# Kernel tuning notes

Hardware: AMD Instinct MI355X
Metric: run time of the kernel (lower is better)

The kernel has to match this reference:

```python
import jax, jax.numpy as jnp
import numpy as np

N_QUBITS = 12
LAYERS = 2
DEPTH = 6
MULTIPLIER = np.pi - np.finfo(np.float32).eps
C = jnp.complex64

# CNOT as a (2,2,2,2) tensor: out[c',t',c,t]
CNOT = jnp.array([[1, 0, 0, 0],
                  [0, 1, 0, 0],
                  [0, 0, 0, 1],
                  [0, 0, 1, 0]], dtype=C).reshape(2, 2, 2, 2)


def _ry(t):
    c, s = jnp.cos(t / 2), jnp.sin(t / 2)
    return jnp.stack([jnp.stack([c, -s]), jnp.stack([s, c])]).astype(C)


def _rz(t):
    e = jnp.exp(-0.5j * t)
    z = jnp.zeros((), C)
    return jnp.stack([jnp.stack([e, z]), jnp.stack([z, jnp.conj(e)])])


def _rot(phi, theta, omega):
    # PennyLane Rot(phi, theta, omega) = RZ(omega) @ RY(theta) @ RZ(phi)
    return _rz(omega) @ _ry(theta) @ _rz(phi)


def _apply_1q(psi, U, w):
    psi = jnp.tensordot(U, psi, axes=([1], [w]))
    return jnp.moveaxis(psi, 0, w)


def _apply_2q(psi, U, c, t):
    psi = jnp.tensordot(U, psi, axes=([2, 3], [c, t]))
    return jnp.moveaxis(psi, (0, 1), (c, t))


def _circuit(x, w):
    # x: (12,) angles; w: (depth, 12, 3) StronglyEntanglingLayers weights
    psi = jnp.zeros((2,) * N_QUBITS, C).at[(0,) * N_QUBITS].set(1.0)
    # AngleEmbedding with rotation='Y'
    for q in range(N_QUBITS):
        psi = _apply_1q(psi, _ry(x[q]), q)
    # StronglyEntanglingLayers: Rot on each wire, then CNOT ring with range r
    depth = w.shape[0]
    for l in range(depth):
        r = l % (N_QUBITS - 1) + 1  # default ranges in PennyLane
        for q in range(N_QUBITS):
            psi = _apply_1q(psi, _rot(w[l, q, 0], w[l, q, 1], w[l, q, 2]), q)
        for q in range(N_QUBITS):
            psi = _apply_2q(psi, CNOT, q, (q + r) % N_QUBITS)
    probs = jnp.real(psi * jnp.conj(psi))  # (2,)*12
    outs = []
    for q in range(N_QUBITS):
        m = probs.sum(axis=tuple(i for i in range(N_QUBITS) if i != q))  # (2,)
        outs.append(m[0] - m[1])  # <Z_q>
    return jnp.stack(outs).astype(jnp.float32)  # (12,)


_vqc = jax.vmap(_circuit, in_axes=(0, None))  # (B,12),(D,12,3) -> (B,12)


def setup_inputs() -> dict:
    key = jax.random.key(0)
    k1, k2 = jax.random.split(key)
    x_ = jax.random.normal(k1, (4096, N_QUBITS), dtype=jnp.float32)
    theta = 0.01 * jax.random.normal(k2, (LAYERS, DEPTH, N_QUBITS, 3), dtype=jnp.float32)
    return {"x_": x_, "theta": theta}


def reference(x_, theta):
    H = x_
    for i in range(theta.shape[0]):
        H = _vqc(H, theta[i])  # (B, 12) expvals, fed back as angles
    return H[:, 3:9] * jnp.float32(MULTIPLIER)
```

## Files before the change

kernel.cpp:

```cpp
#include <hip/hip_runtime.h>
#include <math.h>

#define NQ 12
#define MULT 3.1415925343968237f

typedef _Float16 f16x8 __attribute__((ext_vector_type(8)));
typedef _Float16 f16x2 __attribute__((ext_vector_type(2)));
typedef float f32x4 __attribute__((ext_vector_type(4)));

static __device__ __forceinline__ unsigned int pkh(float a, float b) {
    auto h = __builtin_amdgcn_cvt_pkrtz(a, b);
    return __builtin_bit_cast(unsigned int, h);
}

__host__ __device__ constexpr int cnotf(int s, int r) {
    for (int q = 0; q < NQ; ++q) {
        int tq = q + r; if (tq >= NQ) tq -= NQ;
        s ^= ((s >> (11 - q)) & 1) << (11 - tq);
    }
    return s;
}

__host__ __device__ constexpr int wordL(int I, int u, int n) {
    int I2 = (I >> 2) & 1, I3 = (I >> 3) & 1;
    int u0 = u & 1, u1 = (u >> 1) & 1, u2 = (u >> 2) & 1, u3 = (u >> 3) & 1;
    int n0 = n & 1, n1 = (n >> 1) & 1, n2 = (n >> 2) & 1, n3 = (n >> 3) & 1;
    return (I & 3) | ((I2 ^ u1 ^ n0) << 2) | ((I3 ^ u2 ^ n1) << 3) |
           ((I2 ^ u2 ^ n2) << 4) | (u0 << 5) | (u3 << 6) | (n0 << 7) |
           (n1 << 8) | (n2 << 9) | (n3 << 10) | (u1 << 11);
}

__global__ void vqc_prep(const float* __restrict__ th, _Float16* __restrict__ frag,
                         int* __restrict__ ptabd) {
    int gid = blockIdx.x * 256 + threadIdx.x;
    int job = gid >> 6, lane = gid & 63;
    if (job < 72) {
        int pg = job >> 1, R = job & 1;
        int layer = pg / 18, rem = pg % 18, depth = rem / 3, ph = rem % 3;
        float g[4][2][2][2];
        for (int j = 0; j < 4; ++j) {
            int q = 4 * ph + j;
            const float* w = th + (((layer * 6 + depth) * 12 + q) * 3);
            float phi = w[0], tht = w[1], om = w[2];
            float st, ct, spo, cpo, smo, cmo;
            sincosf(0.5f * tht, &st, &ct);
            sincosf(0.5f * (phi + om), &spo, &cpo);
            sincosf(0.5f * (phi - om), &smo, &cmo);
            g[j][0][0][0] = ct * cpo;  g[j][0][0][1] = -ct * spo;
            g[j][0][1][0] = -st * cmo; g[j][0][1][1] = -st * smo;
            g[j][1][0][0] = st * cmo;  g[j][1][0][1] = -st * smo;
            g[j][1][1][0] = ct * cpo;  g[j][1][1][1] = ct * spo;
        }
        int m = 16 * R + (lane & 15);
        int u = m >> 1, v = m & 1;
        float Wr[4], Wi[4];
        for (int c = 0; c < 4; ++c) {
            int up = (lane >> 4) * 4 + c;
            float ar = 1.f, ai = 0.f;
            for (int j = 0; j < 4; ++j) {
                int ub = (u >> (3 - j)) & 1, vb = (up >> (3 - j)) & 1;
                float gr = g[j][ub][vb][0], gi = g[j][ub][vb][1];
                float nr = ar * gr - ai * gi, ni = ar * gi + ai * gr;
                ar = nr; ai = ni;
            }
            Wr[c] = ar; Wi[c] = ai;
        }
        _Float16* o = frag + ((size_t)job * 64 + lane) * 8;
        for (int i = 0; i < 8; ++i) {
            int c = i >> 1, vp = i & 1;
            float val = (v == vp) ? Wr[c] : (v == 0 ? -Wi[c] : Wi[c]);
            o[i] = (_Float16)val;
        }
    }
    if (blockIdx.x == 0 && threadIdx.x < 72) {
        int d = threadIdx.x / 12, bb = threadIdx.x % 12;
        int sp = cnotf(1 << bb, d + 1);
        ptabd[threadIdx.x] = wordL((sp >> 8) & 15, sp & 15, (sp >> 4) & 15);
    }
}

__global__ __launch_bounds__(256, 4) void vqc_main(
        const float* __restrict__ x, const uint4* __restrict__ frag,
        const int* __restrict__ ptabd, float* __restrict__ out, int nst) {
    __shared__ __align__(16) unsigned int sbuf[8192];
    __shared__ float ang[64];
    const int t = threadIdx.x, lane = t & 63, wv = t >> 6, b = blockIdx.x;
    if (b >= nst) return;

    const int rbase = wordL(4 * (lane >> 4), 4 * wv, lane & 15);
    const int wbase = wordL(lane & 15, 2 * (lane >> 4), 4 * wv);
    constexpr int RC[4] = {wordL(0,0,0), wordL(0,1,0), wordL(0,2,0), wordL(0,3,0)};
    constexpr int WCt[4] = {wordL(0,0,0), wordL(0,0,1), wordL(0,0,2), wordL(0,0,3)};

    int cur = 0;
    float myang = 0.f;
#pragma unroll 1
    for (int l = 0; l < 2; ++l) {
        if (l == 0) { if (lane < NQ) myang = x[b * NQ + lane]; }
        else        { if (lane < NQ) myang = ang[48 + lane]; }
        float sv, cv;
        sincosf(0.5f * myang, &sv, &cv);
        float cq[NQ], sq[NQ];
#pragma unroll
        for (int q = 0; q < NQ; ++q) { cq[q] = __shfl(cv, q, 64); sq[q] = __shfl(sv, q, 64); }
        __syncthreads();

        {
            float Pn = 1.f;
#pragma unroll
            for (int j = 0; j < 4; ++j) Pn *= ((lane >> j) & 1) ? sq[7 - j] : cq[7 - j];
            float Phi = (((lane >> 4) & 1) ? sq[1] : cq[1]) * (((lane >> 4) & 2) ? sq[0] : cq[0]);
            float pre = Pn * Phi;
            float Plo0 = cq[3] * cq[2], Plo1 = sq[3] * cq[2];
            float Plo2 = cq[3] * sq[2], Plo3 = sq[3] * sq[2];
#pragma unroll
            for (int t2 = 0; t2 < 4; ++t2) {
                float Pu = ((t2 & 1) ? sq[11] : cq[11]) * ((t2 & 2) ? sq[10] : cq[10]) *
                           ((wv & 1) ? sq[9] : cq[9]) * ((wv & 2) ? sq[8] : cq[8]);
                float base = pre * Pu;
                uint4 w;
                w.x = pkh(base * Plo0, 0.f);
                w.y = pkh(base * Plo1, 0.f);
                w.z = pkh(base * Plo2, 0.f);
                w.w = pkh(base * Plo3, 0.f);
                *(uint4*)&sbuf[cur * 4096 + (rbase ^ RC[t2])] = w;
            }
        }
        __syncthreads();

#pragma unroll 1
        for (int d = 0; d < 6; ++d) {
            const int* pdp = ptabd + d * 12;
            int p0 = pdp[0], p1 = pdp[1], p2 = pdp[2], p3 = pdp[3];
            int p4 = pdp[4], p5 = pdp[5], p6 = pdp[6], p7 = pdp[7];
            int p8 = pdp[8], p9 = pdp[9], p10 = pdp[10], p11 = pdp[11];
            int pb = 0;
            if (lane & 1)  pb ^= p8;
            if (lane & 2)  pb ^= p9;
            if (lane & 4)  pb ^= p10;
            if (lane & 8)  pb ^= p11;
            if (lane & 16) pb ^= p1;
            if (lane & 32) pb ^= p2;
            if (wv & 1)    pb ^= p6;
            if (wv & 2)    pb ^= p7;
#pragma unroll
            for (int ph = 0; ph < 3; ++ph) {
                const int pg = (l * 6 + d) * 3 + ph;
                f16x8 a0 = __builtin_bit_cast(f16x8, frag[(pg * 2 + 0) * 64 + lane]);
                f16x8 a1 = __builtin_bit_cast(f16x8, frag[(pg * 2 + 1) * 64 + lane]);
                const unsigned int* rp = sbuf + cur * 4096;
                f32x4 zero = {0.f, 0.f, 0.f, 0.f};
                f32x4 ac[2][4];
#pragma unroll
                for (int t2 = 0; t2 < 4; ++t2) {
                    f16x8 bf = __builtin_bit_cast(f16x8, *(const uint4*)&rp[rbase ^ RC[t2]]);
                    ac[0][t2] = __builtin_amdgcn_mfma_f32_16x16x32_f16(a0, bf, zero, 0, 0, 0);
                    ac[1][t2] = __builtin_amdgcn_mfma_f32_16x16x32_f16(a1, bf, zero, 0, 0, 0);
                }
                unsigned int* wp = sbuf + (cur ^ 1) * 4096;
                if (ph < 2) {
#pragma unroll
                    for (int R = 0; R < 2; ++R)
#pragma unroll
                        for (int t2 = 0; t2 < 4; ++t2)
#pragma unroll
                            for (int pr = 0; pr < 2; ++pr) {
                                int word = wbase ^ (32 * pr + 64 * R) ^ WCt[t2];
                                wp[word] = pkh(ac[R][t2][2 * pr], ac[R][t2][2 * pr + 1]);
                            }
                } else {
#pragma unroll
                    for (int R = 0; R < 2; ++R)
#pragma unroll
                        for (int t2 = 0; t2 < 4; ++t2)
#pragma unroll
                            for (int pr = 0; pr < 2; ++pr) {
                                int sc = (R ? p3 : 0) ^ (pr ? p0 : 0) ^
                                         ((t2 & 1) ? p4 : 0) ^ ((t2 & 2) ? p5 : 0);
                                int word = pb ^ sc;
                                wp[word] = pkh(ac[R][t2][2 * pr], ac[R][t2][2 * pr + 1]);
                            }
                }
                __syncthreads();
                cur ^= 1;
            }
        }

        {
            const unsigned int* rp = sbuf + cur * 4096;
            float P = 0.f, e2 = 0.f, e3 = 0.f, Tt[4];
#pragma unroll
            for (int t2 = 0; t2 < 4; ++t2) {
                uint4 v = *(const uint4*)&rp[rbase ^ RC[t2]];
                unsigned int arr[4] = {v.x, v.y, v.z, v.w};
                float tl = 0.f;
#pragma unroll
                for (int i = 0; i < 4; ++i) {
                    f16x2 h = __builtin_bit_cast(f16x2, arr[i]);
                    float re = (float)h[0], im = (float)h[1];
                    float p = re * re + im * im;
                    tl += p;
                    e2 += (i & 2) ? -p : p;
                    e3 += (i & 1) ? -p : p;
                }
                Tt[t2] = tl; P += tl;
            }
            float r[12];
            r[0] = (lane & 32) ? -P : P;
            r[1] = (lane & 16) ? -P : P;
            r[2] = e2; r[3] = e3;
            r[4] = (lane & 8) ? -P : P;
            r[5] = (lane & 4) ? -P : P;
            r[6] = (lane & 2) ? -P : P;
            r[7] = (lane & 1) ? -P : P;
            r[8] = Tt[0]; r[9] = Tt[1]; r[10] = Tt[2]; r[11] = Tt[3];
#pragma unroll
            for (int k = 0; k < 12; ++k) {
#pragma unroll
                for (int m = 1; m < 64; m <<= 1) r[k] += __shfl_xor(r[k], m, 64);
            }
            if (lane == 0) {
#pragma unroll
                for (int k = 0; k < 12; ++k) ang[wv * 12 + k] = r[k];
            }
            __syncthreads();
            if (t < NQ) {
                float E = 0.f;
                if (t < 8) {
                    E = ang[t] + ang[12 + t] + ang[24 + t] + ang[36 + t];
                } else {
#pragma unroll
                    for (int wvi = 0; wvi < 4; ++wvi)
#pragma unroll
                        for (int t2 = 0; t2 < 4; ++t2) {
                            float v = ang[wvi * 12 + 8 + t2];
                            int Tg = 4 * wvi + t2;
                            int bit = (t == 8) ? ((Tg >> 3) & 1) : (t == 9) ? ((Tg >> 2) & 1)
                                    : (t == 10) ? ((Tg >> 1) & 1) : (Tg & 1);
                            E += bit ? -v : v;
                        }
                }
                if (l == 0) ang[48 + t] = E;
                else if (t >= 3 && t < 9) out[b * 6 + (t - 3)] = E * MULT;
            }
            __syncthreads();
        }
    }
}

extern "C" void kernel_launch(void* const* d_in, const int* in_sizes, int n_in,
                              void* d_out, int out_size, void* d_ws, size_t ws_size,
                              hipStream_t stream) {
    const float* x = (const float*)d_in[0];
    const float* th = (const float*)d_in[1];
    float* outp = (float*)d_out;
    _Float16* fragh = (_Float16*)d_ws;
    int* ptabd = (int*)((char*)d_ws + 73728);

    int batch = in_sizes[0] / NQ;

    hipLaunchKernelGGL(vqc_prep, dim3(18), dim3(256), 0, stream, th, fragh, ptabd);
    hipLaunchKernelGGL(vqc_main, dim3(batch), dim3(256), 0, stream, x,
                       (const uint4*)fragh, ptabd, outp, batch);
}
```

Before: 171.6 us.

## Assign one wavefront per sample to eliminate block-level barriers

Each 64-lane wavefront now simulates a whole 4096-amplitude state by itself, instead of four waves sharing one state. This removes every __syncthreads and the ping-pong double buffer, so the state is updated in place after all 16 chunks are read into registers. The cross-wave reduction through shared memory is replaced by register selects. The cost is 16 KB of LDS per sample and much higher register pressure (ow[16][4] plus the 16 accumulator chunks), which is why launch_bounds drops to 2 blocks per CU. That lowers occupancy and may lengthen each wave's serial critical path.

```diff
diff --git a/kernel.cpp b/kernel.cpp
--- a/kernel.cpp
+++ b/kernel.cpp
@@ -79,31 +79,37 @@
     }
 }
 
-__global__ __launch_bounds__(256, 4) void vqc_main(
+__global__ __launch_bounds__(256, 2) void vqc_main(
         const float* __restrict__ x, const uint4* __restrict__ frag,
         const int* __restrict__ ptabd, float* __restrict__ out, int nst) {
-    __shared__ __align__(16) unsigned int sbuf[8192];
-    __shared__ float ang[64];
-    const int t = threadIdx.x, lane = t & 63, wv = t >> 6, b = blockIdx.x;
+    __shared__ __align__(16) unsigned int sbuf[16384];
+    const int t = threadIdx.x, lane = t & 63, wv = t >> 6;
+    const int b = blockIdx.x * 4 + wv;
     if (b >= nst) return;
-
-    const int rbase = wordL(4 * (lane >> 4), 4 * wv, lane & 15);
-    const int wbase = wordL(lane & 15, 2 * (lane >> 4), 4 * wv);
-    constexpr int RC[4] = {wordL(0,0,0), wordL(0,1,0), wordL(0,2,0), wordL(0,3,0)};
-    constexpr int WCt[4] = {wordL(0,0,0), wordL(0,0,1), wordL(0,0,2), wordL(0,0,3)};
-
-    int cur = 0;
+    unsigned int* sl = sbuf + (wv << 12);
+
+    const int rbase0 = wordL(4 * (lane >> 4), 0, lane & 15);
+    const int wbase0 = wordL(lane & 15, 2 * (lane >> 4), 0);
+    constexpr int UC[16] = {
+        wordL(0,0,0),  wordL(0,1,0),  wordL(0,2,0),  wordL(0,3,0),
+        wordL(0,4,0),  wordL(0,5,0),  wordL(0,6,0),  wordL(0,7,0),
+        wordL(0,8,0),  wordL(0,9,0),  wordL(0,10,0), wordL(0,11,0),
+        wordL(0,12,0), wordL(0,13,0), wordL(0,14,0), wordL(0,15,0)};
+    constexpr int WCN[16] = {
+        wordL(0,0,0),  wordL(0,0,1),  wordL(0,0,2),  wordL(0,0,3),
+        wordL(0,0,4),  wordL(0,0,5),  wordL(0,0,6),  wordL(0,0,7),
+        wordL(0,0,8),  wordL(0,0,9),  wordL(0,0,10), wordL(0,0,11),
+        wordL(0,0,12), wordL(0,0,13), wordL(0,0,14), wordL(0,0,15)};
+
     float myang = 0.f;
 #pragma unroll 1
     for (int l = 0; l < 2; ++l) {
-        if (l == 0) { if (lane < NQ) myang = x[b * NQ + lane]; }
-        else        { if (lane < NQ) myang = ang[48 + lane]; }
+        if (l == 0) myang = (lane < NQ) ? x[b * NQ + lane] : 0.f;
         float sv, cv;
         sincosf(0.5f * myang, &sv, &cv);
         float cq[NQ], sq[NQ];
 #pragma unroll
         for (int q = 0; q < NQ; ++q) { cq[q] = __shfl(cv, q, 64); sq[q] = __shfl(sv, q, 64); }
-        __syncthreads();
 
         {
             float Pn = 1.f;
@@ -114,19 +120,18 @@
             float Plo0 = cq[3] * cq[2], Plo1 = sq[3] * cq[2];
             float Plo2 = cq[3] * sq[2], Plo3 = sq[3] * sq[2];
 #pragma unroll
-            for (int t2 = 0; t2 < 4; ++t2) {
-                float Pu = ((t2 & 1) ? sq[11] : cq[11]) * ((t2 & 2) ? sq[10] : cq[10]) *
-                           ((wv & 1) ? sq[9] : cq[9]) * ((wv & 2) ? sq[8] : cq[8]);
+            for (int c = 0; c < 16; ++c) {
+                float Pu = ((c & 1) ? sq[11] : cq[11]) * ((c & 2) ? sq[10] : cq[10]) *
+                           ((c & 4) ? sq[9] : cq[9]) * ((c & 8) ? sq[8] : cq[8]);
                 float base = pre * Pu;
                 uint4 w;
                 w.x = pkh(base * Plo0, 0.f);
                 w.y = pkh(base * Plo1, 0.f);
                 w.z = pkh(base * Plo2, 0.f);
                 w.w = pkh(base * Plo3, 0.f);
-                *(uint4*)&sbuf[cur * 4096 + (rbase ^ RC[t2])] = w;
-            }
-        }
-        __syncthreads();
+                *(uint4*)&sl[rbase0 ^ UC[c]] = w;
+            }
+        }
 
 #pragma unroll 1
         for (int d = 0; d < 6; ++d) {
@@ -134,64 +139,60 @@
             int p0 = pdp[0], p1 = pdp[1], p2 = pdp[2], p3 = pdp[3];
             int p4 = pdp[4], p5 = pdp[5], p6 = pdp[6], p7 = pdp[7];
             int p8 = pdp[8], p9 = pdp[9], p10 = pdp[10], p11 = pdp[11];
-            int pb = 0;
-            if (lane & 1)  pb ^= p8;
-            if (lane & 2)  pb ^= p9;
-            if (lane & 4)  pb ^= p10;
-            if (lane & 8)  pb ^= p11;
-            if (lane & 16) pb ^= p1;
-            if (lane & 32) pb ^= p2;
-            if (wv & 1)    pb ^= p6;
-            if (wv & 2)    pb ^= p7;
-#pragma unroll
+            int pbL = 0;
+            if (lane & 1)  pbL ^= p8;
+            if (lane & 2)  pbL ^= p9;
+            if (lane & 4)  pbL ^= p10;
+            if (lane & 8)  pbL ^= p11;
+            if (lane & 16) pbL ^= p1;
+            if (lane & 32) pbL ^= p2;
+#pragma unroll 1
             for (int ph = 0; ph < 3; ++ph) {
                 const int pg = (l * 6 + d) * 3 + ph;
                 f16x8 a0 = __builtin_bit_cast(f16x8, frag[(pg * 2 + 0) * 64 + lane]);
                 f16x8 a1 = __builtin_bit_cast(f16x8, frag[(pg * 2 + 1) * 64 + lane]);
-                const unsigned int* rp = sbuf + cur * 4096;
                 f32x4 zero = {0.f, 0.f, 0.f, 0.f};
-                f32x4 ac[2][4];
-#pragma unroll
-                for (int t2 = 0; t2 < 4; ++t2) {
-                    f16x8 bf = __builtin_bit_cast(f16x8, *(const uint4*)&rp[rbase ^ RC[t2]]);
-                    ac[0][t2] = __builtin_amdgcn_mfma_f32_16x16x32_f16(a0, bf, zero, 0, 0, 0);
-                    ac[1][t2] = __builtin_amdgcn_mfma_f32_16x16x32_f16(a1, bf, zero, 0, 0, 0);
-                }
-                unsigned int* wp = sbuf + (cur ^ 1) * 4096;
+                unsigned int ow[16][4];
+#pragma unroll
+                for (int c = 0; c < 16; ++c) {
+                    f16x8 bf = __builtin_bit_cast(f16x8, *(const uint4*)&sl[rbase0 ^ UC[c]]);
+                    f32x4 ac0 = __builtin_amdgcn_mfma_f32_16x16x32_f16(a0, bf, zero, 0, 0, 0);
+                    f32x4 ac1 = __builtin_amdgcn_mfma_f32_16x16x32_f16(a1, bf, zero, 0, 0, 0);
+                    ow[c][0] = pkh(ac0[0], ac0[1]);
+                    ow[c][1] = pkh(ac0[2], ac0[3]);
+                    ow[c][2] = pkh(ac1[0], ac1[1]);
+                    ow[c][3] = pkh(ac1[2], ac1[3]);
+                }
                 if (ph < 2) {
 #pragma unroll
-                    for (int R = 0; R < 2; ++R)
-#pragma unroll
-                        for (int t2 = 0; t2 < 4; ++t2)
-#pragma unroll
-                            for (int pr = 0; pr < 2; ++pr) {
-                                int word = wbase ^ (32 * pr + 64 * R) ^ WCt[t2];
-                                wp[word] = pkh(ac[R][t2][2 * pr], ac[R][t2][2 * pr + 1]);
-                            }
+                    for (int c = 0; c < 16; ++c) {
+                        int wb = wbase0 ^ WCN[c];
+                        sl[wb]      = ow[c][0];
+                        sl[wb ^ 32] = ow[c][1];
+                        sl[wb ^ 64] = ow[c][2];
+                        sl[wb ^ 96] = ow[c][3];
+                    }
                 } else {
 #pragma unroll
-                    for (int R = 0; R < 2; ++R)
-#pragma unroll
-                        for (int t2 = 0; t2 < 4; ++t2)
-#pragma unroll
-                            for (int pr = 0; pr < 2; ++pr) {
-                                int sc = (R ? p3 : 0) ^ (pr ? p0 : 0) ^
-                                         ((t2 & 1) ? p4 : 0) ^ ((t2 & 2) ? p5 : 0);
-                                int word = pb ^ sc;
-                                wp[word] = pkh(ac[R][t2][2 * pr], ac[R][t2][2 * pr + 1]);
-                            }
-                }
-                __syncthreads();
-                cur ^= 1;
+                    for (int c = 0; c < 16; ++c) {
+                        int pcc = ((c & 1) ? p4 : 0) ^ ((c & 2) ? p5 : 0) ^
+                                  ((c & 4) ? p6 : 0) ^ ((c & 8) ? p7 : 0);
+                        int wb = pbL ^ pcc;
+                        sl[wb]           = ow[c][0];
+                        sl[wb ^ p0]      = ow[c][1];
+                        sl[wb ^ p3]      = ow[c][2];
+                        sl[wb ^ p3 ^ p0] = ow[c][3];
+                    }
+                }
             }
         }
 
         {
-            const unsigned int* rp = sbuf + cur * 4096;
-            float P = 0.f, e2 = 0.f, e3 = 0.f, Tt[4];
-#pragma unroll
-            for (int t2 = 0; t2 < 4; ++t2) {
-                uint4 v = *(const uint4*)&rp[rbase ^ RC[t2]];
+            float P = 0.f, e2 = 0.f, e3 = 0.f;
+            float t8 = 0.f, t9 = 0.f, t10 = 0.f, t11 = 0.f;
+#pragma unroll
+            for (int c = 0; c < 16; ++c) {
+                uint4 v = *(const uint4*)&sl[rbase0 ^ UC[c]];
                 unsigned int arr[4] = {v.x, v.y, v.z, v.w};
                 float tl = 0.f;
 #pragma unroll
@@ -203,7 +204,11 @@
                     e2 += (i & 2) ? -p : p;
                     e3 += (i & 1) ? -p : p;
                 }
-                Tt[t2] = tl; P += tl;
+                P += tl;
+                t8  += (c & 8) ? -tl : tl;
+                t9  += (c & 4) ? -tl : tl;
+                t10 += (c & 2) ? -tl : tl;
+                t11 += (c & 1) ? -tl : tl;
             }
             float r[12];
             r[0] = (lane & 32) ? -P : P;
@@ -213,37 +218,24 @@
             r[5] = (lane & 4) ? -P : P;
             r[6] = (lane & 2) ? -P : P;
             r[7] = (lane & 1) ? -P : P;
-            r[8] = Tt[0]; r[9] = Tt[1]; r[10] = Tt[2]; r[11] = Tt[3];
+            r[8] = t8; r[9] = t9; r[10] = t10; r[11] = t11;
 #pragma unroll
             for (int k = 0; k < 12; ++k) {
 #pragma unroll
                 for (int m = 1; m < 64; m <<= 1) r[k] += __shfl_xor(r[k], m, 64);
             }
-            if (lane == 0) {
-#pragma unroll
-                for (int k = 0; k < 12; ++k) ang[wv * 12 + k] = r[k];
-            }
-            __syncthreads();
-            if (t < NQ) {
-                float E = 0.f;
-                if (t < 8) {
-                    E = ang[t] + ang[12 + t] + ang[24 + t] + ang[36 + t];
-                } else {
-#pragma unroll
-                    for (int wvi = 0; wvi < 4; ++wvi)
-#pragma unroll
-                        for (int t2 = 0; t2 < 4; ++t2) {
-                            float v = ang[wvi * 12 + 8 + t2];
-                            int Tg = 4 * wvi + t2;
-                            int bit = (t == 8) ? ((Tg >> 3) & 1) : (t == 9) ? ((Tg >> 2) & 1)
-                                    : (t == 10) ? ((Tg >> 1) & 1) : (Tg & 1);
-                            E += bit ? -v : v;
-                        }
-                }
-                if (l == 0) ang[48 + t] = E;
-                else if (t >= 3 && t < 9) out[b * 6 + (t - 3)] = E * MULT;
-            }
-            __syncthreads();
+            if (l == 0) {
+                myang = (lane == 0) ? r[0] : (lane == 1) ? r[1] : (lane == 2) ? r[2] :
+                        (lane == 3) ? r[3] : (lane == 4) ? r[4] : (lane == 5) ? r[5] :
+                        (lane == 6) ? r[6] : (lane == 7) ? r[7] : (lane == 8) ? r[8] :
+                        (lane == 9) ? r[9] : (lane == 10) ? r[10] : (lane == 11) ? r[11] : 0.f;
+            } else {
+                if (lane >= 3 && lane < 9) {
+                    float v = (lane == 3) ? r[3] : (lane == 4) ? r[4] : (lane == 5) ? r[5] :
+                              (lane == 6) ? r[6] : (lane == 7) ? r[7] : r[8];
+                    out[b * 6 + (lane - 3)] = v * MULT;
+                }
+            }
         }
     }
 }
@@ -258,8 +250,9 @@
     int* ptabd = (int*)((char*)d_ws + 73728);
 
     int batch = in_sizes[0] / NQ;
+    int blocks = (batch + 3) / 4;
 
     hipLaunchKernelGGL(vqc_prep, dim3(18), dim3(256), 0, stream, th, fragh, ptabd);
-    hipLaunchKernelGGL(vqc_main, dim3(batch), dim3(256), 0, stream, x,
+    hipLaunchKernelGGL(vqc_main, dim3(blocks), dim3(256), 0, stream, x,
                        (const uint4*)fragh, ptabd, outp, batch);
 }
```

After: 176.1 us. 2.6% more time.
